# Optimization experiments

Measured on AMD Instinct MI355X. Metric: run time of the kernel, lower is better.

Reference implementation:

```python
import jax, jax.numpy as jnp
import numpy as np
from jax.scipy.linalg import solve_triangular

EPS = 1e-5
CHUNK = 64

def _rms(x, w, eps=EPS):
    return x * jax.lax.rsqrt(jnp.mean(x * x, axis=-1, keepdims=True) + eps) * w

def _l2norm(x, eps=1e-6):
    return x * jax.lax.rsqrt(jnp.sum(x * x, axis=-1, keepdims=True) + eps)

def _causal_conv(x, w):
    # x: [B,T,C], w: [C,K] depthwise causal short conv
    K = w.shape[1]
    T = x.shape[1]
    xp = jnp.pad(x, ((0, 0), (K - 1, 0), (0, 0)))
    return sum(xp[:, j:j + T, :] * w[:, j] for j in range(K))

def _chunk_gated_delta_rule(q, k, v, g, beta, chunk=CHUNK):
    # q,k: [B,H,T,Dk] (l2-normalized, q pre-scaled); v: [B,H,T,Dv]; g,beta: [B,H,T]
    Bb, H, T, Dk = k.shape
    Dv = v.shape[-1]
    N = T // chunk
    qc, kc, vc = (a.reshape(Bb, H, N, chunk, -1) for a in (q, k, v))
    gc = g.reshape(Bb, H, N, chunk)
    bc = beta.reshape(Bb, H, N, chunk)
    gcs = jnp.cumsum(gc, axis=-1)  # within-chunk cumulative log-decay
    tri = jnp.tril(jnp.ones((chunk, chunk), bool))
    tri_s = jnp.tril(jnp.ones((chunk, chunk), bool), -1)
    diff = gcs[..., :, None] - gcs[..., None, :]
    decay = jnp.where(tri, jnp.exp(jnp.where(tri, diff, 0.0)), 0.0)  # [B,H,N,C,C]
    k_beta = kc * bc[..., None]
    v_beta = vc * bc[..., None]
    A = jnp.einsum('bhnck,bhndk->bhncd', k_beta, kc) * decay
    A = jnp.where(tri_s, A, 0.0)
    eye = jnp.eye(chunk, dtype=q.dtype)
    Tmat = solve_triangular(eye + A, jnp.broadcast_to(eye, A.shape), lower=True)  # (I+A)^-1
    u = Tmat @ v_beta                               # [B,H,N,C,Dv]
    w = Tmat @ (k_beta * jnp.exp(gcs)[..., None])   # [B,H,N,C,Dk]

    def step(S, inp):
        q_i, k_i, u_i, w_i, g_i, dm_i = inp
        attn = jnp.where(tri, jnp.einsum('bhck,bhdk->bhcd', q_i, k_i) * dm_i, 0.0)
        v_new = u_i - w_i @ S
        o_i = (q_i * jnp.exp(g_i)[..., None]) @ S + attn @ v_new
        g_last = g_i[..., -1]
        k_dec = k_i * jnp.exp(g_last[..., None] - g_i)[..., None]
        S = S * jnp.exp(g_last)[..., None, None] + jnp.einsum('bhck,bhcv->bhkv', k_dec, v_new)
        return S, o_i

    xs = tuple(jnp.moveaxis(a, 2, 0) for a in (qc, kc, u, w, gcs, decay))
    S0 = jnp.zeros((Bb, H, Dk, Dv), q.dtype)
    _, outs = jax.lax.scan(step, S0, xs)  # [N,B,H,C,Dv]
    return jnp.moveaxis(outs, 0, 2).reshape(Bb, H, T, Dv)

def _layer_forward(x, mask, ln1_w, qkvz_w, ba_w, conv_w, A_log, dt_bias,
                   o_norm_w, out_w, ln2_w, gate_w, up_w, down_w):
    B, T, D = x.shape
    H = A_log.shape[0]
    kd = qkvz_w.shape[0] // 4  # key_dim == value_dim here (k_heads==v_heads, Dk==Dv)
    vd = kd
    Dk = kd // H
    Dv = vd // H
    silu = jax.nn.silu
    h = _rms(x, ln1_w)
    qkvz = h @ qkvz_w.T
    q, k, v, z = jnp.split(qkvz, [kd, 2 * kd, 2 * kd + vd], axis=-1)
    b, a = jnp.split(h @ ba_w.T, 2, axis=-1)  # [B,T,H] each
    mixed = jnp.concatenate([q, k, v], axis=-1) * mask[..., None]
    mixed = silu(_causal_conv(mixed, conv_w))
    q, k, v = jnp.split(mixed, [kd, 2 * kd], axis=-1)
    q = _l2norm(q.reshape(B, T, H, Dk))
    k = _l2norm(k.reshape(B, T, H, Dk))
    v = v.reshape(B, T, H, Dv)
    beta = jax.nn.sigmoid(b) * mask[..., None]
    g = -jnp.exp(A_log) * jax.nn.softplus(a + dt_bias) * mask[..., None]
    scale = Dk ** -0.5
    bhtd = lambda t: jnp.transpose(t, (0, 2, 1, 3))
    o = _chunk_gated_delta_rule(bhtd(q) * scale, bhtd(k), bhtd(v),
                                jnp.transpose(g, (0, 2, 1)), jnp.transpose(beta, (0, 2, 1)))
    o = jnp.transpose(o, (0, 2, 1, 3))  # [B,T,H,Dv]
    o = _rms(o, o_norm_w) * silu(z.reshape(B, T, H, Dv))  # gated RMSNorm
    x = x + o.reshape(B, T, vd) @ out_w.T
    h2 = _rms(x, ln2_w)
    mlp_out = (silu(h2 @ gate_w.T) * (h2 @ up_w.T)) @ down_w.T
    return x + mlp_out

def setup_inputs():
    key = jax.random.key(0)
    ks = jax.random.split(key, 12)
    B, T, D, H, Dk, Dv, M, K = 1, 4096, 2048, 16, 128, 128, 8192, 4
    kd, vd = H * Dk, H * Dv
    nrm = lambda i, shp, sc=0.02: jax.random.normal(ks[i], shp, jnp.float32) * sc
    return {
        'x': nrm(0, (B, T, D), 1.0),
        'mask': jnp.ones((B, T), jnp.float32),
        'ln1_w': jnp.ones((D,), jnp.float32),
        'qkvz_w': nrm(1, (2 * kd + 2 * vd, D)),
        'ba_w': nrm(2, (2 * H, D)),
        'conv_w': nrm(3, (2 * kd + vd, K), 0.3),
        'A_log': jnp.log(jax.random.uniform(ks[4], (H,), jnp.float32, 1.0, 16.0)),
        'dt_bias': nrm(5, (H,), 0.5),
        'o_norm_w': jnp.ones((Dv,), jnp.float32),
        'out_w': nrm(6, (D, vd)),
        'ln2_w': jnp.ones((D,), jnp.float32),
        'gate_w': nrm(7, (M, D)),
        'up_w': nrm(8, (M, D)),
        'down_w': nrm(9, (D, M)),
    }

def reference(x, mask, ln1_w, qkvz_w, ba_w, conv_w, A_log, dt_bias,
              o_norm_w, out_w, ln2_w, gate_w, up_w, down_w):
    return _layer_forward(x, mask, ln1_w, qkvz_w, ba_w, conv_w, A_log, dt_bias,
                          o_norm_w, out_w, ln2_w, gate_w, up_w, down_w)
```

## Files before the change

kernel.cpp:

```cpp
#include <hip/hip_runtime.h>
#include <math.h>

#define T_LEN 4096
#define DMODEL 2048
#define NH 16
#define CQKV 6144
#define CQKVZ 8192
#define SCALE 0.08838834764831845f

using bf16x8 = __attribute__((ext_vector_type(8))) short;
using f32x4  = __attribute__((ext_vector_type(4))) float;

__device__ __forceinline__ float siluf(float x) { return x / (1.0f + __expf(-x)); }

__device__ __forceinline__ unsigned short f2bf(float f) {
  unsigned int u = __float_as_uint(f);
  u = (u + 0x7FFFu + ((u >> 16) & 1u)) >> 16;
  return (unsigned short)u;
}
__device__ __forceinline__ float bf2f(unsigned short u) {
  return __uint_as_float(((unsigned int)u) << 16);
}
__device__ __forceinline__ ushort4 pack4(float a, float b, float c, float d) {
  ushort4 r; r.x = f2bf(a); r.y = f2bf(b); r.z = f2bf(c); r.w = f2bf(d); return r;
}

__device__ __forceinline__ void gl_lds16(const unsigned short* g, unsigned short* l) {
  __builtin_amdgcn_global_load_lds(
      (const __attribute__((address_space(1))) void*)g,
      (__attribute__((address_space(3))) void*)l, 16, 0, 0);
}

template<int MODE>
__global__ __launch_bounds__(256) void rmsnorm_kernel(const float* __restrict__ x,
                                                      const float* __restrict__ w,
                                                      float* __restrict__ outf,
                                                      unsigned short* __restrict__ outb) {
  const int t = blockIdx.x;
  const int tid = threadIdx.x;
  const float4* xr = (const float4*)(x + (size_t)t * DMODEL);
  float4 v0 = xr[tid];
  float4 v1 = xr[tid + 256];
  float s = v0.x*v0.x + v0.y*v0.y + v0.z*v0.z + v0.w*v0.w
          + v1.x*v1.x + v1.y*v1.y + v1.z*v1.z + v1.w*v1.w;
#pragma unroll
  for (int off = 32; off > 0; off >>= 1) s += __shfl_down(s, off);
  __shared__ float red[4];
  if ((tid & 63) == 0) red[tid >> 6] = s;
  __syncthreads();
  const float tot = red[0] + red[1] + red[2] + red[3];
  const float r = rsqrtf(tot * (1.0f / DMODEL) + 1e-5f);
  const float4* wr = (const float4*)w;
  const float4 w0 = wr[tid], w1 = wr[tid + 256];
  float4 o0, o1;
  o0.x = v0.x*r*w0.x; o0.y = v0.y*r*w0.y; o0.z = v0.z*r*w0.z; o0.w = v0.w*r*w0.w;
  o1.x = v1.x*r*w1.x; o1.y = v1.y*r*w1.y; o1.z = v1.z*r*w1.z; o1.w = v1.w*r*w1.w;
  if (MODE == 1) {
    float4* orow = (float4*)(outf + (size_t)t * DMODEL);
    orow[tid] = o0;
    orow[tid + 256] = o1;
  }
  ushort4* brow = (ushort4*)(outb + (size_t)t * DMODEL);
  brow[tid] = pack4(o0.x, o0.y, o0.z, o0.w);
  brow[tid + 256] = pack4(o1.x, o1.y, o1.z, o1.w);
}

__global__ __launch_bounds__(256) void f2b_kernel(const float* __restrict__ in,
                                                  unsigned short* __restrict__ out) {
  const size_t i = (size_t)blockIdx.x * 256 + threadIdx.x;
  const float4 a = ((const float4*)in)[2 * i];
  const float4 b = ((const float4*)in)[2 * i + 1];
  ((ushort4*)out)[2 * i] = pack4(a.x, a.y, a.z, a.w);
  ((ushort4*)out)[2 * i + 1] = pack4(b.x, b.y, b.z, b.w);
}

template<int EPI>
__global__ __launch_bounds__(512, 2) void gemm8p_kernel(const unsigned short* __restrict__ A,
                                                        const unsigned short* __restrict__ B,
                                                        float* __restrict__ Cf,
                                                        unsigned short* __restrict__ Cb,
                                                        unsigned short* __restrict__ Zb,
                                                        int M, int N, int K) {
  __shared__ __align__(16) unsigned short lds[8][8192];
  const int nbm = M >> 8, nbn = N >> 8, nwg = nbm * nbn;
  const int nt = K >> 6;
  int bmi, bni;
  {
    const int bid = blockIdx.x;
    const int cpx = nwg >> 3;
    int sc = 1;
    while (sc * sc < cpx) sc <<= 1;
    if (sc * sc > cpx) sc >>= 1;
    const int scn = (sc > 0) ? (cpx / sc) : 0;
    if ((nwg & 7) == 0 && sc > 0 && sc * scn == cpx && (nbm % sc) == 0 && (nbn % scn) == 0) {
      const int chunk = bid & 7, widx = bid >> 3;
      const int regc = nbn / scn;
      bmi = (chunk / regc) * sc + widx / scn;
      bni = (chunk % regc) * scn + widx % scn;
    } else {
      bmi = bid / nbn; bni = bid % nbn;
    }
  }
  const int bm = bmi << 8, bn = bni << 8;
  const int tid = threadIdx.x;
  const int wv = tid >> 6, ln = tid & 63;
  const int fr = ln & 15, qq = ln >> 4;
  const int wm = wv >> 2, wn = wv & 3;
  const int rsw = (fr >> 1) & 3;
  const int s_sl = (ln & 3) ^ ((ln >> 3) & 3);

  f32x4 acc[8][4];
  const f32x4 zero = {0.f, 0.f, 0.f, 0.f};
#pragma unroll
  for (int mf = 0; mf < 8; mf++)
#pragma unroll
    for (int nf = 0; nf < 4; nf++) acc[mf][nf] = zero;

  bf16x8 afr[8], bfr[2];

  auto stage_half = [&](int t2, int part) {
    if (t2 >= nt) return;
    const unsigned short* Mat = (part >= 2) ? B : A;
    const int gb = (part >= 2) ? bn : bm;
    const int kk = part & 1;
    const int slot = ((t2 & 1) << 2) | part;
    const int k0 = t2 * 64 + kk * 32;
#pragma unroll
    for (int q = 0; q < 2; q++) {
      gl_lds16(Mat + (size_t)(gb + wv * 32 + q * 16 + (ln >> 2)) * K + k0 + s_sl * 8,
               &lds[slot][(wv * 32 + q * 16) * 32]);
    }
  };
  auto lda = [&](int tb, int kk) {
#pragma unroll
    for (int mf = 0; mf < 8; mf++) {
      const int ar = wm * 128 + mf * 16 + fr;
      afr[mf] = *(const bf16x8*)&lds[tb | kk][ar * 32 + ((qq ^ rsw) << 3)];
    }
  };
  auto ldb = [&](int tb, int kk, int nh) {
#pragma unroll
    for (int nj = 0; nj < 2; nj++) {
      const int br = wn * 64 + (nh * 2 + nj) * 16 + fr;
      bfr[nj] = *(const bf16x8*)&lds[tb | (2 + kk)][br * 32 + ((qq ^ rsw) << 3)];
    }
  };
  auto mm = [&](int nh) {
    __builtin_amdgcn_s_setprio(1);
#pragma unroll
    for (int mf = 0; mf < 8; mf++)
#pragma unroll
      for (int nj = 0; nj < 2; nj++)
        acc[mf][nh * 2 + nj] =
            __builtin_amdgcn_mfma_f32_16x16x32_bf16(afr[mf], bfr[nj], acc[mf][nh * 2 + nj], 0, 0, 0);
    __builtin_amdgcn_s_setprio(0);
  };

  stage_half(0, 0); stage_half(0, 2); stage_half(0, 1); stage_half(0, 3);
  stage_half(1, 0); stage_half(1, 2);
  asm volatile("s_waitcnt vmcnt(4)" ::: "memory");
  __builtin_amdgcn_s_barrier();
  asm volatile("" ::: "memory");

  for (int t = 0; t < nt; t++) {
    const int tb = (t & 1) << 2;
    lda(tb, 0); ldb(tb, 0, 0);
    stage_half(t + 1, 1);
    __builtin_amdgcn_s_barrier();
    mm(0);
    __builtin_amdgcn_s_barrier();
    ldb(tb, 0, 1);
    stage_half(t + 1, 3);
    __builtin_amdgcn_s_barrier();
    mm(1);
    __builtin_amdgcn_s_barrier();
    lda(tb, 1); ldb(tb, 1, 1);
    stage_half(t + 2, 0);
    __builtin_amdgcn_s_barrier();
    mm(1);
    __builtin_amdgcn_s_barrier();
    ldb(tb, 1, 0);
    stage_half(t + 2, 2);
    __builtin_amdgcn_s_barrier();
    mm(0);
    if (t + 1 < nt) {
      asm volatile("s_waitcnt lgkmcnt(0)" ::: "memory");
      __builtin_amdgcn_sched_barrier(0);
      if (t == nt - 2) {
        asm volatile("s_waitcnt vmcnt(0)" ::: "memory");
      } else {
        asm volatile("s_waitcnt vmcnt(4)" ::: "memory");
      }
      __builtin_amdgcn_sched_barrier(0);
      __builtin_amdgcn_s_barrier();
      __builtin_amdgcn_sched_barrier(0);
    }
  }

  const int cm4 = qq * 4;
  if (EPI == 3) {
    const int bn2 = bn >> 1;
#pragma unroll
    for (int mf = 0; mf < 8; mf++) {
#pragma unroll
      for (int p = 0; p < 2; p++) {
#pragma unroll
        for (int r = 0; r < 4; r++) {
          const int grow = bm + wm * 128 + mf * 16 + cm4 + r;
          const int gcol = bn2 + wn * 32 + p * 16 + fr;
          Cb[(size_t)grow * 8192 + gcol] =
              f2bf(siluf(acc[mf][2 * p][r]) * acc[mf][2 * p + 1][r]);
        }
      }
    }
  } else {
    const bool isZ = (Zb != nullptr) && (bn >= CQKV);
#pragma unroll
    for (int mf = 0; mf < 8; mf++) {
#pragma unroll
      for (int nf = 0; nf < 4; nf++) {
#pragma unroll
        for (int r = 0; r < 4; r++) {
          const int grow = bm + wm * 128 + mf * 16 + cm4 + r;
          const int gcol = bn + wn * 64 + nf * 16 + fr;
          const float v = acc[mf][nf][r];
          if (EPI == 0) {
            const unsigned short bv = f2bf(v);
            if (isZ) Zb[(size_t)grow * 2048 + (gcol - CQKV)] = bv;
            else     Cb[(size_t)grow * N + gcol] = bv;
          } else {
            Cf[(size_t)grow * N + gcol] += v;
          }
        }
      }
    }
  }
}

template<int EPI, int BM, int BN>
__global__ __launch_bounds__(512, 4) void gemm256_kernel(const unsigned short* __restrict__ A,
                                                         const unsigned short* __restrict__ B,
                                                         float* __restrict__ Cf,
                                                         const float* __restrict__ Xres,
                                                         int M, int N, int K) {
  constexpr int MI = 4;
  constexpr int NI = BN / 64;
  constexpr int AW = BM / 128;
  constexpr int BW = BN / 128;
  __shared__ __align__(16) unsigned short lds[3][(BM + BN) * 32];
  const int nbm = M / BM, nbn = N / BN, nwg = nbm * nbn;
  const int nt = K >> 5;
  int bmi, bni;
  {
    const int bid = blockIdx.x;
    const int cpx = nwg >> 3;
    int sc = 1;
    while (sc * sc < cpx) sc <<= 1;
    if (sc * sc > cpx) sc >>= 1;
    const int scn = (sc > 0) ? (cpx / sc) : 0;
    if ((nwg & 7) == 0 && sc > 0 && sc * scn == cpx && (nbm % sc) == 0 && (nbn % scn) == 0) {
      const int chunk = bid & 7, widx = bid >> 3;
      const int regc = nbn / scn;
      bmi = (chunk / regc) * sc + widx / scn;
      bni = (chunk % regc) * scn + widx % scn;
    } else {
      bmi = bid / nbn; bni = bid % nbn;
    }
  }
  const int bm = bmi * BM, bn = bni * BN;
  const int tid = threadIdx.x;
  const int wv = tid >> 6, ln = tid & 63;
  const int fr = ln & 15, qq = ln >> 4;
  const int wm = wv >> 2, wn = wv & 3;
  const int ra0 = wm * 64, rb0 = wn * (BN / 4);
  const int lrow = ln >> 2;
  const int lslot = ln & 3;

  f32x4 acc[MI][NI];
  const f32x4 zero = {0.f, 0.f, 0.f, 0.f};
#pragma unroll
  for (int mi = 0; mi < MI; mi++)
#pragma unroll
    for (int ni = 0; ni < NI; ni++) acc[mi][ni] = zero;

  auto stage = [&](int buf, int t) {
    const int k0 = t << 5;
#pragma unroll
    for (int q = 0; q < AW; q++) {
      const int lr = q * 128 + wv * 16 + lrow;
      const int sl = lslot ^ ((lr >> 1) & 3);
      gl_lds16(A + (size_t)(bm + lr) * K + k0 + sl * 8,
               &lds[buf][(q * 128 + wv * 16) * 32]);
    }
#pragma unroll
    for (int q = 0; q < BW; q++) {
      const int lr = q * 128 + wv * 16 + lrow;
      const int sl = lslot ^ ((lr >> 1) & 3);
      gl_lds16(B + (size_t)(bn + lr) * K + k0 + sl * 8,
               &lds[buf][BM * 32 + (q * 128 + wv * 16) * 32]);
    }
  };

  stage(0, 0);
  stage(1, 1);
  asm volatile("s_waitcnt vmcnt(%0)" :: "i"(AW + BW) : "memory");
  __builtin_amdgcn_s_barrier();
  asm volatile("" ::: "memory");

  for (int t = 0; t < nt; t++) {
    const int cb = t % 3;
    const int b2 = (t + 2) % 3;
    const unsigned short* lA = &lds[cb][0];
    const unsigned short* lB = &lds[cb][BM * 32];
    bf16x8 bfr[NI];
#pragma unroll
    for (int ni = 0; ni < NI; ni++) {
      const int r = rb0 + ni * 16 + fr;
      bfr[ni] = *(const bf16x8*)&lB[r * 32 + ((qq ^ ((r >> 1) & 3)) << 3)];
    }
    bf16x8 afr[MI];
#pragma unroll
    for (int mi = 0; mi < MI; mi++) {
      const int r = ra0 + mi * 16 + fr;
      afr[mi] = *(const bf16x8*)&lA[r * 32 + ((qq ^ ((r >> 1) & 3)) << 3)];
    }
    if (t + 2 < nt) stage(b2, t + 2);
    __builtin_amdgcn_s_setprio(1);
#pragma unroll
    for (int mi = 0; mi < MI; mi++)
#pragma unroll
      for (int ni = 0; ni < NI; ni++)
        acc[mi][ni] = __builtin_amdgcn_mfma_f32_16x16x32_bf16(afr[mi], bfr[ni], acc[mi][ni], 0, 0, 0);
    __builtin_amdgcn_s_setprio(0);
    if (t + 1 < nt) {
      asm volatile("s_waitcnt lgkmcnt(0)" ::: "memory");
      if (t + 2 < nt) {
        asm volatile("s_waitcnt vmcnt(%0)" :: "i"(AW + BW) : "memory");
      } else {
        asm volatile("s_waitcnt vmcnt(0)" ::: "memory");
      }
      __builtin_amdgcn_s_barrier();
      asm volatile("" ::: "memory");
    }
  }

  const int cm4 = qq * 4;
#pragma unroll
  for (int mi = 0; mi < MI; mi++) {
#pragma unroll
    for (int ni = 0; ni < NI; ni++) {
#pragma unroll
      for (int r = 0; r < 4; r++) {
        const int grow = bm + ra0 + mi * 16 + cm4 + r;
        const int gcol = bn + rb0 + ni * 16 + fr;
        const size_t off = (size_t)grow * N + gcol;
        const float v = acc[mi][ni][r];
        if (EPI == 1) {
          Cf[off] += v;
        } else {
          Cf[off] = Xres[off] + v;
        }
      }
    }
  }
}

__global__ __launch_bounds__(256) void ba_gemm_kernel(const unsigned short* __restrict__ h_in,
                                                      const float* __restrict__ ba_w,
                                                      float* __restrict__ ba_out) {
  __shared__ __align__(16) float hl[2048];
  __shared__ float red[32][9];
  const int t = blockIdx.x;
  const int tid = threadIdx.x;
  union { uint4 u; unsigned short s[8]; } wv_;
  wv_.u = *(const uint4*)(h_in + (size_t)t * DMODEL + tid * 8);
#pragma unroll
  for (int j = 0; j < 8; j++) hl[tid * 8 + j] = bf2f(wv_.s[j]);
  __syncthreads();
  const int c = tid & 31;
  const int p = tid >> 5;
  const float* wrow = ba_w + (size_t)c * DMODEL + p * 256;
  const float* hrow = hl + p * 256;
  float s = 0.f;
#pragma unroll 8
  for (int k = 0; k < 256; k++) s += hrow[k] * wrow[k];
  red[c][p] = s;
  __syncthreads();
  if (tid < 32) {
    float tot = 0.f;
#pragma unroll
    for (int q = 0; q < 8; q++) tot += red[tid][q];
    ba_out[(size_t)t * 32 + tid] = tot;
  }
}

__global__ __launch_bounds__(256) void conv_norm_kernel(const unsigned short* __restrict__ qkvz,
                                                        const float* __restrict__ conv_w,
                                                        const float* __restrict__ mask,
                                                        unsigned short* __restrict__ mixed) {
  __shared__ float vals[6144];
  const int t = blockIdx.x;
  const int tid = threadIdx.x;
  float mj[4];
#pragma unroll
  for (int j = 0; j < 4; j++) {
    const int tt = t - 3 + j;
    mj[j] = (tt >= 0) ? mask[tt] : 0.f;
  }
#pragma unroll
  for (int p = 0; p < 6; p++) {
    const int c4 = (p * 256 + tid) * 4;
    const float4 w0 = *(const float4*)(conv_w + (size_t)c4 * 4);
    const float4 w1 = *(const float4*)(conv_w + (size_t)c4 * 4 + 4);
    const float4 w2 = *(const float4*)(conv_w + (size_t)c4 * 4 + 8);
    const float4 w3 = *(const float4*)(conv_w + (size_t)c4 * 4 + 12);
    const float wj0[4] = {w0.x, w0.y, w0.z, w0.w};
    const float wj1[4] = {w1.x, w1.y, w1.z, w1.w};
    const float wj2[4] = {w2.x, w2.y, w2.z, w2.w};
    const float wj3[4] = {w3.x, w3.y, w3.z, w3.w};
    float4 acc = make_float4(0.f, 0.f, 0.f, 0.f);
#pragma unroll
    for (int j = 0; j < 4; j++) {
      const int tt = t - 3 + j;
      if (tt < 0) continue;
      const ushort4 xb = *(const ushort4*)(qkvz + (size_t)tt * CQKVZ + c4);
      acc.x += bf2f(xb.x) * mj[j] * wj0[j];
      acc.y += bf2f(xb.y) * mj[j] * wj1[j];
      acc.z += bf2f(xb.z) * mj[j] * wj2[j];
      acc.w += bf2f(xb.w) * mj[j] * wj3[j];
    }
    vals[c4]     = siluf(acc.x);
    vals[c4 + 1] = siluf(acc.y);
    vals[c4 + 2] = siluf(acc.z);
    vals[c4 + 3] = siluf(acc.w);
  }
  __syncthreads();
  unsigned short* orow = mixed + (size_t)t * CQKV;
  const int hh = tid >> 3;
  const int li = tid & 7;
  const int base = hh * 128 + li * 16;
  float loc[16];
  float s = 0.f;
#pragma unroll
  for (int j = 0; j < 16; j++) { loc[j] = vals[base + j]; s += loc[j] * loc[j]; }
#pragma unroll
  for (int msk = 1; msk < 8; msk <<= 1) s += __shfl_xor(s, msk);
  const float rn = rsqrtf(s + 1e-6f);
#pragma unroll
  for (int j8 = 0; j8 < 2; j8++) {
    *(ushort4*)(orow + base + j8 * 8) =
        pack4(loc[j8*8+0]*rn, loc[j8*8+1]*rn, loc[j8*8+2]*rn, loc[j8*8+3]*rn);
    *(ushort4*)(orow + base + j8 * 8 + 4) =
        pack4(loc[j8*8+4]*rn, loc[j8*8+5]*rn, loc[j8*8+6]*rn, loc[j8*8+7]*rn);
  }
  const int vc = 4096 + tid * 8;
  *(ushort4*)(orow + vc) = pack4(vals[vc], vals[vc+1], vals[vc+2], vals[vc+3]);
  *(ushort4*)(orow + vc + 4) = pack4(vals[vc+4], vals[vc+5], vals[vc+6], vals[vc+7]);
}

__global__ __launch_bounds__(256) void beta_g_kernel(const float* __restrict__ ba,
                                                     const float* __restrict__ A_log,
                                                     const float* __restrict__ dt_bias,
                                                     const float* __restrict__ mask,
                                                     float* __restrict__ beta,
                                                     float* __restrict__ g) {
  const int idx = blockIdx.x * 256 + threadIdx.x;
  const int t = idx >> 4;
  const int h = idx & 15;
  const float b = ba[(size_t)t * 32 + h];
  const float a = ba[(size_t)t * 32 + 16 + h];
  const float m = mask[t];
  beta[idx] = m / (1.0f + expf(-b));
  const float xx = a + dt_bias[h];
  const float sp = (xx > 20.0f) ? xx : log1pf(expf(xx));
  g[idx] = -expf(A_log[h]) * sp * m;
}

__global__ __launch_bounds__(256) void gcs_kernel(const float* __restrict__ g,
                                                  float* __restrict__ gcsbuf,
                                                  float* __restrict__ edkbuf,
                                                  float* __restrict__ egqbuf,
                                                  float* __restrict__ adecbuf) {
  const int idx = blockIdx.x * 256 + threadIdx.x;
  if (idx >= 1024) return;
  const int h = idx >> 6;
  const int n = idx & 63;
  const int t0 = n * 64;
  float s = 0.f;
  for (int i = 0; i < 64; i++) {
    s += g[(size_t)(t0 + i) * NH + h];
    gcsbuf[(size_t)idx * 64 + i] = s;
  }
  const float glast = s;
  adecbuf[idx] = __expf(glast);
  for (int i = 0; i < 64; i++) {
    const float gi = gcsbuf[(size_t)idx * 64 + i];
    edkbuf[(size_t)idx * 64 + i] = __expf(glast - gi);
    egqbuf[(size_t)idx * 64 + i] = __expf(gi) * SCALE;
  }
}

__global__ __launch_bounds__(256) void pre_attn_kernel(const unsigned short* __restrict__ mixed,
                                                       const float* __restrict__ gcsbuf,
                                                       const float* __restrict__ betabuf,
                                                       float* __restrict__ abuf,
                                                       unsigned short* __restrict__ attnb) {
  __shared__ __align__(16) unsigned short kbl[64 * 128];
  __shared__ __align__(16) unsigned short qbl[64 * 128];
  __shared__ float gcs_s[64];
  __shared__ float betal[64];
  const int blk = blockIdx.x;
  const int h = blk >> 6;
  const int n = blk & 63;
  const int t0 = n * 64;
  const int tid = threadIdx.x;
  if (tid < 64) {
    gcs_s[tid] = gcsbuf[(size_t)blk * 64 + tid];
    betal[tid] = betabuf[(size_t)(t0 + tid) * NH + h];
  }
#pragma unroll
  for (int p = 0; p < 4; p++) {
    const int idx = tid + p * 256;
    const int i = idx >> 4, dg = idx & 15;
    *(uint4*)&kbl[i * 128 + ((dg ^ (i & 7)) << 3)] =
        *(const uint4*)(mixed + (size_t)(t0 + i) * CQKV + 2048 + h * 128 + dg * 8);
    *(uint4*)&qbl[i * 128 + ((dg ^ (i & 7)) << 3)] =
        *(const uint4*)(mixed + (size_t)(t0 + i) * CQKV + h * 128 + dg * 8);
  }
  __syncthreads();
  const int ln = tid & 63;
  const int wv = tid >> 6;
  const int fr = ln & 15;
  const int g = ln >> 4;
  const int i0 = wv * 16;
  f32x4 accA[4], accQ[4];
  const f32x4 zero = {0.f, 0.f, 0.f, 0.f};
#pragma unroll
  for (int jt = 0; jt < 4; jt++) { accA[jt] = zero; accQ[jt] = zero; }
#pragma unroll
  for (int ks = 0; ks < 4; ks++) {
    const int kb = ks * 4 + g;
    const int ar = i0 + fr;
    const bf16x8 aK = *(const bf16x8*)&kbl[ar * 128 + ((kb ^ (ar & 7)) << 3)];
    const bf16x8 aQ = *(const bf16x8*)&qbl[ar * 128 + ((kb ^ (ar & 7)) << 3)];
#pragma unroll
    for (int jt = 0; jt < 4; jt++) {
      const int br = jt * 16 + fr;
      const bf16x8 b = *(const bf16x8*)&kbl[br * 128 + ((kb ^ (br & 7)) << 3)];
      accA[jt] = __builtin_amdgcn_mfma_f32_16x16x32_bf16(aK, b, accA[jt], 0, 0, 0);
      accQ[jt] = __builtin_amdgcn_mfma_f32_16x16x32_bf16(aQ, b, accQ[jt], 0, 0, 0);
    }
  }
#pragma unroll
  for (int jt = 0; jt < 4; jt++) {
    const int j = jt * 16 + fr;
    const float gj = gcs_s[j];
#pragma unroll
    for (int r = 0; r < 4; r++) {
      const int i = i0 + g * 4 + r;
      const float gi = gcs_s[i];
      const float dec = __expf(fminf(gi - gj, 0.f));
      abuf[(size_t)blk * 4096 + i * 64 + j] = (i > j) ? accA[jt][r] * betal[i] * dec : 0.f;
      attnb[(size_t)blk * 4096 + i * 64 + j] =
          f2bf((i >= j) ? accQ[jt][r] * dec * SCALE : 0.f);
    }
  }
}

__global__ __launch_bounds__(256) void pre_solve_kernel(const float* __restrict__ abuf,
                                                        const float* __restrict__ betabuf,
                                                        float* __restrict__ tbuf) {
  __shared__ float Al[64][65];
  __shared__ float Tl[64][65];
  const int blk = blockIdx.x;
  const int h = blk >> 6;
  const int n = blk & 63;
  const int t0 = n * 64;
  const int tid = threadIdx.x;
#pragma unroll
  for (int rep = 0; rep < 4; rep++) {
    const int lin = rep * 256 + tid;
    const int i = lin >> 4;
    const int j = (lin & 15) * 4;
    const float4 av = *(const float4*)(abuf + (size_t)blk * 4096 + i * 64 + j);
    Al[i][j] = av.x; Al[i][j + 1] = av.y; Al[i][j + 2] = av.z; Al[i][j + 3] = av.w;
  }
  __syncthreads();
  if (tid < 64) {
    const int j = tid;
    const float bj = betabuf[(size_t)(t0 + j) * NH + h];
    for (int i = 0; i < 64; i++) {
      float s = (i == j) ? 1.0f : 0.0f;
      for (int l = j; l < i; l++) s -= Al[i][l] * Tl[l][j];
      Tl[i][j] = s;
    }
    for (int i = j; i < 64; i++) Tl[i][j] *= bj;
  }
  __syncthreads();
#pragma unroll
  for (int rep = 0; rep < 4; rep++) {
    const int lin = rep * 256 + tid;
    const int i = lin >> 4;
    const int j = (lin & 15) * 4;
    float4 tv;
    tv.x = Tl[i][j]; tv.y = Tl[i][j + 1]; tv.z = Tl[i][j + 2]; tv.w = Tl[i][j + 3];
    *(float4*)(tbuf + (size_t)blk * 4096 + i * 64 + j) = tv;
  }
}

__global__ __launch_bounds__(256) void pre_uw_kernel(const unsigned short* __restrict__ mixed,
                                                     const float* __restrict__ tbuf,
                                                     const float* __restrict__ gcsbuf,
                                                     unsigned short* __restrict__ ubf,
                                                     unsigned short* __restrict__ wbf) {
  __shared__ __align__(16) float Tl[64][68];
  __shared__ __align__(16) float xl[64][132];
  __shared__ float egcs[64];
  const int blk = blockIdx.x;
  const int h = blk >> 6;
  const int n = blk & 63;
  const int t0 = n * 64;
  const int tid = threadIdx.x;
  if (tid < 64) egcs[tid] = __expf(gcsbuf[(size_t)blk * 64 + tid]);
#pragma unroll
  for (int rep = 0; rep < 4; rep++) {
    const int lin = rep * 256 + tid;
    const int i = lin >> 4;
    const int j = (lin & 15) * 4;
    const float4 tv = *(const float4*)(tbuf + (size_t)blk * 4096 + i * 64 + j);
    *(float4*)&Tl[i][j] = tv;
  }
#pragma unroll
  for (int rep = 0; rep < 4; rep++) {
    const int lin = rep * 256 + tid;
    const int i = lin >> 4;
    const int d8 = (lin & 15) * 8;
    union { uint4 u; unsigned short s[8]; } w;
    w.u = *(const uint4*)(mixed + (size_t)(t0 + i) * CQKV + 4096 + h * 128 + d8);
#pragma unroll
    for (int j = 0; j < 8; j++) xl[i][d8 + j] = bf2f(w.s[j]);
  }
  __syncthreads();
  const int cgu = tid & 15;
  const int riu = tid >> 4;
  const int i0 = riu * 4;
  const int d0 = cgu * 8;
  float acc[4][8];
#pragma unroll
  for (int a = 0; a < 4; a++)
#pragma unroll
    for (int b = 0; b < 8; b++) acc[a][b] = 0.f;
#pragma unroll 2
  for (int j = 0; j < 64; j++) {
    const float tv[4] = {Tl[i0][j], Tl[i0 + 1][j], Tl[i0 + 2][j], Tl[i0 + 3][j]};
    const float4 x0 = *(const float4*)&xl[j][d0];
    const float4 x1 = *(const float4*)&xl[j][d0 + 4];
    const float xv[8] = {x0.x, x0.y, x0.z, x0.w, x1.x, x1.y, x1.z, x1.w};
#pragma unroll
    for (int a = 0; a < 4; a++)
#pragma unroll
      for (int b = 0; b < 8; b++) acc[a][b] += tv[a] * xv[b];
  }
#pragma unroll
  for (int b = 0; b < 8; b++) {
    *(ushort4*)(ubf + (size_t)blk * 8192 + riu * 512 + (size_t)(d0 + b) * 4) =
        pack4(acc[0][b], acc[1][b], acc[2][b], acc[3][b]);
  }
  __syncthreads();
#pragma unroll
  for (int rep = 0; rep < 4; rep++) {
    const int lin = rep * 256 + tid;
    const int i = lin >> 4;
    const int d8 = (lin & 15) * 8;
    union { uint4 u; unsigned short s[8]; } w;
    w.u = *(const uint4*)(mixed + (size_t)(t0 + i) * CQKV + 2048 + h * 128 + d8);
    const float e = egcs[i];
#pragma unroll
    for (int j = 0; j < 8; j++) xl[i][d8 + j] = bf2f(w.s[j]) * e;
  }
  __syncthreads();
#pragma unroll
  for (int a = 0; a < 4; a++)
#pragma unroll
    for (int b = 0; b < 8; b++) acc[a][b] = 0.f;
#pragma unroll 2
  for (int j = 0; j < 64; j++) {
    const float tv[4] = {Tl[i0][j], Tl[i0 + 1][j], Tl[i0 + 2][j], Tl[i0 + 3][j]};
    const float4 x0 = *(const float4*)&xl[j][d0];
    const float4 x1 = *(const float4*)&xl[j][d0 + 4];
    const float xv[8] = {x0.x, x0.y, x0.z, x0.w, x1.x, x1.y, x1.z, x1.w};
#pragma unroll
    for (int a = 0; a < 4; a++)
#pragma unroll
      for (int b = 0; b < 8; b++) acc[a][b] += tv[a] * xv[b];
  }
#pragma unroll
  for (int a = 0; a < 4; a++) {
    const int l = i0 + a;
    unsigned short* wp = wbf + (size_t)(t0 + l) * 2048 + h * 128 + ((cgu ^ (l & 7)) << 3);
    *(ushort4*)wp = pack4(-acc[a][0], -acc[a][1], -acc[a][2], -acc[a][3]);
    *(ushort4*)(wp + 4) = pack4(-acc[a][4], -acc[a][5], -acc[a][6], -acc[a][7]);
  }
}

__global__ __launch_bounds__(256) void ktrans_kernel(const unsigned short* __restrict__ mixed,
                                                     const float* __restrict__ edkbuf,
                                                     const float* __restrict__ egqbuf,
                                                     unsigned short* __restrict__ kdT,
                                                     unsigned short* __restrict__ qe) {
  __shared__ __align__(16) float kl[64][132];
  __shared__ float edk_s[64];
  __shared__ float egq_s[64];
  const int blk = blockIdx.x;
  const int h = blk >> 6;
  const int n = blk & 63;
  const int t0 = n * 64;
  const int tid = threadIdx.x;
  if (tid < 64) {
    edk_s[tid] = edkbuf[(size_t)blk * 64 + tid];
    egq_s[tid] = egqbuf[(size_t)blk * 64 + tid];
  }
#pragma unroll
  for (int q = 0; q < 4; q++) {
    const int idx = tid + q * 256;
    const int l = idx >> 4, d8 = (idx & 15) * 8;
    union { uint4 u; unsigned short s[8]; } w;
    w.u = *(const uint4*)(mixed + (size_t)(t0 + l) * CQKV + 2048 + h * 128 + d8);
#pragma unroll
    for (int j = 0; j < 8; j++) kl[l][d8 + j] = bf2f(w.s[j]);
  }
  __syncthreads();
#pragma unroll
  for (int q = 0; q < 4; q++) {
    const int idx = tid + q * 256;
    const int d = idx >> 3, lsl = idx & 7;
    const int l8 = lsl * 8;
    float v[8];
#pragma unroll
    for (int j = 0; j < 8; j++) v[j] = kl[l8 + j][d] * edk_s[l8 + j];
    unsigned short* p = kdT + (size_t)blk * 8192 + d * 64 + ((lsl ^ (d & 7)) << 3);
    *(ushort4*)p = pack4(v[0], v[1], v[2], v[3]);
    *(ushort4*)(p + 4) = pack4(v[4], v[5], v[6], v[7]);
  }
#pragma unroll
  for (int q = 0; q < 4; q++) {
    const int idx = tid + q * 256;
    const int i = idx >> 4, c8 = (idx & 15) * 8;
    union { uint4 u; unsigned short s[8]; } w;
    w.u = *(const uint4*)(mixed + (size_t)(t0 + i) * CQKV + h * 128 + c8);
    const float e = egq_s[i];
    unsigned short* qp = qe + (size_t)(t0 + i) * 2048 + h * 128 + c8;
    *(ushort4*)qp = pack4(bf2f(w.s[0]) * e, bf2f(w.s[1]) * e, bf2f(w.s[2]) * e, bf2f(w.s[3]) * e);
    *(ushort4*)(qp + 4) = pack4(bf2f(w.s[4]) * e, bf2f(w.s[5]) * e, bf2f(w.s[6]) * e, bf2f(w.s[7]) * e);
  }
}

__global__ __launch_bounds__(512, 1) void scan_kernel(const unsigned short* __restrict__ wbf,
                                                      const unsigned short* __restrict__ kdT,
                                                      const unsigned short* __restrict__ ubf,
                                                      const float* __restrict__ adecbuf,
                                                      unsigned short* __restrict__ STb,
                                                      unsigned short* __restrict__ vtb,
                                                      const float* __restrict__ gw,
                                                      const float* __restrict__ uw,
                                                      const float* __restrict__ dw,
                                                      const float* __restrict__ ow,
                                                      unsigned short* __restrict__ Wgu,
                                                      unsigned short* __restrict__ Wd,
                                                      unsigned short* __restrict__ Wo) {
  __shared__ __align__(16) unsigned short stage[2][16384];
  __shared__ __align__(16) unsigned short privAll[4][3072];
  if (blockIdx.x >= 32) {
    const int xb = blockIdx.x - 32;
    const int tid = threadIdx.x;
    if (xb < 8192) {
      const bool isUp = (xb >= 4096);
      const float* src = isUp ? uw : gw;
      const size_t e = ((size_t)(isUp ? xb - 4096 : xb) * 512 + tid) * 8;
      const int r = (int)(e >> 11);
      const int col = (int)(e & 2047);
      const int drow = (r >> 4) * 32 + (r & 15) + (isUp ? 16 : 0);
      const float4 a = *(const float4*)(src + e);
      const float4 b = *(const float4*)(src + e + 4);
      unsigned short* dst = Wgu + (size_t)drow * 2048 + col;
      *(ushort4*)dst = pack4(a.x, a.y, a.z, a.w);
      *(ushort4*)(dst + 4) = pack4(b.x, b.y, b.z, b.w);
    } else {
      const float* src; unsigned short* dst; size_t u;
      if (xb < 12288) { src = dw; dst = Wd; u = (size_t)(xb - 8192) * 512 + tid; }
      else            { src = ow; dst = Wo; u = (size_t)(xb - 12288) * 512 + tid; }
      const float4 a = ((const float4*)src)[2 * u];
      const float4 b = ((const float4*)src)[2 * u + 1];
      ((ushort4*)dst)[2 * u] = pack4(a.x, a.y, a.z, a.w);
      ((ushort4*)dst)[2 * u + 1] = pack4(b.x, b.y, b.z, b.w);
    }
    return;
  }
  const int h = blockIdx.x >> 1;
  const int chalf = blockIdx.x & 1;
  const int tid = threadIdx.x;
  const int wv = tid >> 6;
  if (wv >= 4) {
    __builtin_amdgcn_s_barrier();
    for (int n = 0; n < 63; n++) __builtin_amdgcn_s_barrier();
    return;
  }
  const int ln = tid & 63;
  const int fr = ln & 15;
  const int g  = ln >> 4;
  const int c0 = chalf * 64 + wv * 16;
  const int fsw = fr & 7;
  unsigned short* privA = &privAll[wv][0];
  unsigned short* privB = &privAll[wv][2048];
  const f32x4 zero = {0.f, 0.f, 0.f, 0.f};

  f32x4 acc2[8];
#pragma unroll
  for (int dt = 0; dt < 8; dt++) acc2[dt] = zero;

  auto stage_wk = [&](int buf, int n1) {
    const int t0n = n1 * 64;
    const size_t kbase = (size_t)(h * 64 + n1) * 8192;
#pragma unroll
    for (int q = 0; q < 4; q++) {
      const int m = wv * 4 + q;
      gl_lds16(wbf + (size_t)(t0n + m * 4 + (ln >> 4)) * 2048 + h * 128 + (ln & 15) * 8,
               &stage[buf][m * 512]);
      gl_lds16(kdT + kbase + (m * 8 + (ln >> 3)) * 64 + (ln & 7) * 8,
               &stage[buf][8192 + m * 512]);
    }
  };

  ushort4 ur4[4];
#pragma unroll
  for (int lt = 0; lt < 4; lt++)
    ur4[lt] = *(const ushort4*)(ubf + (size_t)(h * 64) * 8192 + (lt * 4 + g) * 512 + (c0 + fr) * 4);
  float ad = adecbuf[h * 64];
  stage_wk(0, 0);
  asm volatile("s_waitcnt vmcnt(0)" ::: "memory");
  __builtin_amdgcn_s_barrier();
  asm volatile("" ::: "memory");

  for (int n = 0; n < 64; n++) {
    const int blk = h * 64 + n;
    const unsigned short* wl = &stage[n & 1][0];
    const unsigned short* kl = &stage[n & 1][8192];
    if (n + 1 < 64) stage_wk((n + 1) & 1, n + 1);
    __builtin_amdgcn_sched_barrier(0);
    ushort4 ur4n[4];
    float adn = 0.f;
    if (n + 1 < 64) {
      const size_t ub = (size_t)(blk + 1) * 8192;
#pragma unroll
      for (int lt = 0; lt < 4; lt++)
        ur4n[lt] = *(const ushort4*)(ubf + ub + (lt * 4 + g) * 512 + (c0 + fr) * 4);
      adn = adecbuf[blk + 1];
    } else {
#pragma unroll
      for (int lt = 0; lt < 4; lt++) { ur4n[lt].x = 0; ur4n[lt].y = 0; ur4n[lt].z = 0; ur4n[lt].w = 0; }
    }
    __builtin_amdgcn_sched_barrier(0);
#pragma unroll
    for (int dt = 0; dt < 8; dt++) {
      const int slot = dt * 2 + (g >> 1);
      const ushort4 pv = pack4(acc2[dt][0], acc2[dt][1], acc2[dt][2], acc2[dt][3]);
      *(ushort4*)&privA[fr * 128 + ((slot ^ fsw) << 3) + (g & 1) * 4] = pv;
      *(ushort4*)(STb + (size_t)blk * 16384 + (dt * 4 + g) * 512 + (c0 + fr) * 4) = pv;
    }
    f32x4 acc1[4];
#pragma unroll
    for (int lt = 0; lt < 4; lt++) {
      f32x4 t;
      t[0] = bf2f(ur4[lt].x); t[1] = bf2f(ur4[lt].y);
      t[2] = bf2f(ur4[lt].z); t[3] = bf2f(ur4[lt].w);
      acc1[lt] = t;
    }
#pragma unroll
    for (int ks = 0; ks < 4; ks++) {
      const int kb = ks * 4 + g;
      const bf16x8 b = *(const bf16x8*)&privA[fr * 128 + ((kb ^ fsw) << 3)];
#pragma unroll
      for (int lt = 0; lt < 4; lt++) {
        const bf16x8 a = *(const bf16x8*)&wl[(lt * 16 + fr) * 128 + ((kb ^ fsw) << 3)];
        acc1[lt] = __builtin_amdgcn_mfma_f32_16x16x32_bf16(a, b, acc1[lt], 0, 0, 0);
      }
    }
#pragma unroll
    for (int lt = 0; lt < 4; lt++) {
      const int slot = lt * 2 + (g >> 1);
      const ushort4 pv = pack4(acc1[lt][0], acc1[lt][1], acc1[lt][2], acc1[lt][3]);
      *(ushort4*)&privB[fr * 64 + ((slot ^ fsw) << 3) + (g & 1) * 4] = pv;
      *(ushort4*)(vtb + (size_t)blk * 8192 + (lt * 4 + g) * 512 + (c0 + fr) * 4) = pv;
    }
#pragma unroll
    for (int dt = 0; dt < 8; dt++) {
      acc2[dt][0] *= ad; acc2[dt][1] *= ad; acc2[dt][2] *= ad; acc2[dt][3] *= ad;
    }
#pragma unroll
    for (int ks = 0; ks < 2; ks++) {
      const int kb = ks * 4 + g;
      const bf16x8 b = *(const bf16x8*)&privB[fr * 64 + ((kb ^ fsw) << 3)];
#pragma unroll
      for (int dt = 0; dt < 8; dt++) {
        const bf16x8 a = *(const bf16x8*)&kl[(dt * 16 + fr) * 64 + ((kb ^ fsw) << 3)];
        acc2[dt] = __builtin_amdgcn_mfma_f32_16x16x32_bf16(a, b, acc2[dt], 0, 0, 0);
      }
    }
#pragma unroll
    for (int lt = 0; lt < 4; lt++) ur4[lt] = ur4n[lt];
    ad = adn;
    if (n + 1 < 64) {
      asm volatile("s_waitcnt lgkmcnt(0)" ::: "memory");
      __builtin_amdgcn_sched_barrier(0);
      asm volatile("s_waitcnt vmcnt(17)" ::: "memory");
      __builtin_amdgcn_sched_barrier(0);
      __builtin_amdgcn_s_barrier();
      __builtin_amdgcn_sched_barrier(0);
    }
  }
}

__global__ __launch_bounds__(256) void ocomp_kernel(const unsigned short* __restrict__ qe,
                                                    const unsigned short* __restrict__ STbuf,
                                                    const unsigned short* __restrict__ vtbuf,
                                                    const unsigned short* __restrict__ attnb,
                                                    const unsigned short* __restrict__ zb,
                                                    const float* __restrict__ onw,
                                                    unsigned short* __restrict__ ob) {
  __shared__ __align__(16) unsigned short STl[128 * 128];
  __shared__ __align__(16) unsigned short vtl[128 * 64];
  __shared__ __align__(16) unsigned short ql[64 * 128];
  __shared__ __align__(16) unsigned short al[64 * 64];
  const int blk = blockIdx.x;
  const int h = blk >> 6;
  const int n = blk & 63;
  const int t0 = n * 64;
  const int tid = threadIdx.x;
#pragma unroll
  for (int q = 0; q < 8; q++) {
    const int o = tid + q * 256;
    const int dq = o >> 6, w = o & 63;
    const uint4 v = *(const uint4*)(STbuf + (size_t)blk * 16384 + (size_t)o * 8);
    const int cA = 2 * w, cB = 2 * w + 1;
    uint2 h0; h0.x = v.x; h0.y = v.y;
    uint2 h1; h1.x = v.z; h1.y = v.w;
    *(uint2*)&STl[cA * 128 + (((dq >> 1) ^ (cA & 7)) << 3) + (dq & 1) * 4] = h0;
    *(uint2*)&STl[cB * 128 + (((dq >> 1) ^ (cB & 7)) << 3) + (dq & 1) * 4] = h1;
  }
#pragma unroll
  for (int q = 0; q < 4; q++) {
    const int o = tid + q * 256;
    const int lq = o >> 6, w = o & 63;
    const uint4 v = *(const uint4*)(vtbuf + (size_t)blk * 8192 + (size_t)o * 8);
    const int cA = 2 * w, cB = 2 * w + 1;
    uint2 h0; h0.x = v.x; h0.y = v.y;
    uint2 h1; h1.x = v.z; h1.y = v.w;
    *(uint2*)&vtl[cA * 64 + (((lq >> 1) ^ (cA & 7)) << 3) + (lq & 1) * 4] = h0;
    *(uint2*)&vtl[cB * 64 + (((lq >> 1) ^ (cB & 7)) << 3) + (lq & 1) * 4] = h1;
  }
#pragma unroll
  for (int q = 0; q < 4; q++) {
    const int idx = tid + q * 256;
    const int i = idx >> 4, dg = idx & 15;
    *(uint4*)&ql[i * 128 + ((dg ^ (i & 7)) << 3)] =
        *(const uint4*)(qe + (size_t)(t0 + i) * 2048 + h * 128 + dg * 8);
  }
#pragma unroll
  for (int q = 0; q < 2; q++) {
    const int idx = tid + q * 256;
    const int i = idx >> 3, lsl = idx & 7;
    *(uint4*)&al[i * 64 + ((lsl ^ (i & 7)) << 3)] =
        *(const uint4*)(attnb + (size_t)blk * 4096 + i * 64 + lsl * 8);
  }
  __syncthreads();
  const int ln = tid & 63;
  const int wv = tid >> 6;
  const int fr = ln & 15;
  const int g = ln >> 4;
  const int i0 = wv * 16;
  f32x4 acc[8];
  const f32x4 zero = {0.f, 0.f, 0.f, 0.f};
#pragma unroll
  for (int nt = 0; nt < 8; nt++) acc[nt] = zero;
#pragma unroll
  for (int ks = 0; ks < 4; ks++) {
    const int kb = ks * 4 + g;
    const int ar = i0 + fr;
    const bf16x8 a = *(const bf16x8*)&ql[ar * 128 + ((kb ^ (ar & 7)) << 3)];
#pragma unroll
    for (int nt = 0; nt < 8; nt++) {
      const int c = nt * 16 + fr;
      const bf16x8 b = *(const bf16x8*)&STl[c * 128 + ((kb ^ (c & 7)) << 3)];
      acc[nt] = __builtin_amdgcn_mfma_f32_16x16x32_bf16(a, b, acc[nt], 0, 0, 0);
    }
  }
#pragma unroll
  for (int ks = 0; ks < 2; ks++) {
    const int kb = ks * 4 + g;
    const int ar = i0 + fr;
    const bf16x8 a = *(const bf16x8*)&al[ar * 64 + ((kb ^ (ar & 7)) << 3)];
#pragma unroll
    for (int nt = 0; nt < 8; nt++) {
      const int c = nt * 16 + fr;
      const bf16x8 b = *(const bf16x8*)&vtl[c * 64 + ((kb ^ (c & 7)) << 3)];
      acc[nt] = __builtin_amdgcn_mfma_f32_16x16x32_bf16(a, b, acc[nt], 0, 0, 0);
    }
  }
  float s0 = 0.f, s1 = 0.f, s2 = 0.f, s3 = 0.f;
#pragma unroll
  for (int nt = 0; nt < 8; nt++) {
    s0 += acc[nt][0] * acc[nt][0];
    s1 += acc[nt][1] * acc[nt][1];
    s2 += acc[nt][2] * acc[nt][2];
    s3 += acc[nt][3] * acc[nt][3];
  }
#pragma unroll
  for (int m = 1; m < 16; m <<= 1) {
    s0 += __shfl_xor(s0, m);
    s1 += __shfl_xor(s1, m);
    s2 += __shfl_xor(s2, m);
    s3 += __shfl_xor(s3, m);
  }
  float rn[4];
  rn[0] = rsqrtf(s0 * (1.0f / 128.0f) + 1e-5f);
  rn[1] = rsqrtf(s1 * (1.0f / 128.0f) + 1e-5f);
  rn[2] = rsqrtf(s2 * (1.0f / 128.0f) + 1e-5f);
  rn[3] = rsqrtf(s3 * (1.0f / 128.0f) + 1e-5f);
#pragma unroll
  for (int nt = 0; nt < 8; nt++) {
    const int c = nt * 16 + fr;
    const float wn = onw[c];
#pragma unroll
    for (int r = 0; r < 4; r++) {
      const size_t off = (size_t)(t0 + i0 + g * 4 + r) * 2048 + h * 128 + c;
      const float zz = siluf(bf2f(zb[off]));
      ob[off] = f2bf(acc[nt][r] * rn[r] * wn * zz);
    }
  }
}

extern "C" void kernel_launch(void* const* d_in, const int* in_sizes, int n_in,
                              void* d_out, int out_size, void* d_ws, size_t ws_size,
                              hipStream_t stream) {
  (void)in_sizes; (void)n_in; (void)out_size;
  const float* x        = (const float*)d_in[0];
  const float* mask     = (const float*)d_in[1];
  const float* ln1_w    = (const float*)d_in[2];
  const float* qkvz_w   = (const float*)d_in[3];
  const float* ba_w     = (const float*)d_in[4];
  const float* conv_w   = (const float*)d_in[5];
  const float* A_log    = (const float*)d_in[6];
  const float* dt_bias  = (const float*)d_in[7];
  const float* o_norm_w = (const float*)d_in[8];
  const float* out_w    = (const float*)d_in[9];
  const float* ln2_w    = (const float*)d_in[10];
  const float* gate_w   = (const float*)d_in[11];
  const float* up_w     = (const float*)d_in[12];
  const float* down_w   = (const float*)d_in[13];
  float* out = (float*)d_out;

  const size_t NEED_BYTES = (size_t)75825152 * 4;
  if (ws_size < NEED_BYTES) return;

  float* ws = (float*)d_ws;
  unsigned short* mixed_bf = (unsigned short*)ws;
  unsigned short* Wgu = (unsigned short*)ws;
  unsigned short* Wd = (unsigned short*)(ws + 16777216);
  unsigned short* qkvz_bf = (unsigned short*)(ws + 25165824);
  unsigned short* u_bf = (unsigned short*)(ws + 25165824);
  unsigned short* wbf = (unsigned short*)(ws + 33554432);
  unsigned short* kdT = (unsigned short*)(ws + 37748736);
  unsigned short* comb_bf = (unsigned short*)(ws + 25165824);
  unsigned short* z_bf = (unsigned short*)(ws + 41943040);
  float* a_buf = ws + 46137344;
  unsigned short* vt_buf = (unsigned short*)(ws + 46137344);
  float* t_buf = ws + 50331648;
  unsigned short* qe_bf = (unsigned short*)(ws + 50331648);
  unsigned short* h_bf  = (unsigned short*)(ws + 54525952);
  unsigned short* ob    = (unsigned short*)(ws + 54525952);
  unsigned short* h2_bf = (unsigned short*)(ws + 54525952);
  unsigned short* attn_bf = (unsigned short*)(ws + 58720256);
  unsigned short* Wq = (unsigned short*)(ws + 62914560);
  unsigned short* ST_buf = (unsigned short*)(ws + 62914560);
  unsigned short* Wo = (unsigned short*)(ws + 71303168);
  float* ba_buf   = ws + 73400320;
  float* beta_buf = ws + 73531392;
  float* g_buf    = ws + 73596928;
  float* gcs_buf  = ws + 73662464;
  float* edk_buf  = ws + 73728000;
  float* egq_buf  = ws + 73793536;
  float* adec_buf = ws + 73859072;

  rmsnorm_kernel<2><<<4096, 256, 0, stream>>>(x, ln1_w, nullptr, h_bf);
  f2b_kernel<<<8192, 256, 0, stream>>>(qkvz_w, Wq);
  gemm8p_kernel<0><<<512, 512, 0, stream>>>(h_bf, Wq, nullptr, qkvz_bf, z_bf, 4096, 8192, 2048);
  ba_gemm_kernel<<<4096, 256, 0, stream>>>(h_bf, ba_w, ba_buf);
  conv_norm_kernel<<<4096, 256, 0, stream>>>(qkvz_bf, conv_w, mask, mixed_bf);
  beta_g_kernel<<<256, 256, 0, stream>>>(ba_buf, A_log, dt_bias, mask, beta_buf, g_buf);
  gcs_kernel<<<4, 256, 0, stream>>>(g_buf, gcs_buf, edk_buf, egq_buf, adec_buf);
  pre_attn_kernel<<<1024, 256, 0, stream>>>(mixed_bf, gcs_buf, beta_buf, a_buf, attn_bf);
  pre_solve_kernel<<<1024, 256, 0, stream>>>(a_buf, beta_buf, t_buf);
  pre_uw_kernel<<<1024, 256, 0, stream>>>(mixed_bf, t_buf, gcs_buf, u_bf, wbf);
  ktrans_kernel<<<1024, 256, 0, stream>>>(mixed_bf, edk_buf, egq_buf, kdT, qe_bf);
  scan_kernel<<<13344, 512, 0, stream>>>(wbf, kdT, u_bf, adec_buf, ST_buf, vt_buf,
                                         gate_w, up_w, down_w, out_w,
                                         Wgu, Wd, Wo);
  ocomp_kernel<<<1024, 256, 0, stream>>>(qe_bf, ST_buf, vt_buf, attn_bf,
                                         z_bf, o_norm_w, ob);
  gemm256_kernel<4, 128, 128><<<512, 512, 0, stream>>>(ob, Wo, out, x, 4096, 2048, 2048);
  rmsnorm_kernel<2><<<4096, 256, 0, stream>>>(out, ln2_w, nullptr, h2_bf);
  gemm8p_kernel<3><<<1024, 512, 0, stream>>>(h2_bf, Wgu, nullptr, comb_bf, nullptr, 4096, 16384, 2048);
  gemm256_kernel<1, 128, 128><<<512, 512, 0, stream>>>(comb_bf, Wd, out, nullptr, 4096, 2048, 8192);
}
```

Before: 1.214 ms.

## Fuse triangular solve into u/w kernel and split scan across four blocks per head

```diff
diff --git a/kernel.cpp b/kernel.cpp
--- a/kernel.cpp
+++ b/kernel.cpp
@@ -567,54 +567,14 @@
   }
 }
 
-__global__ __launch_bounds__(256) void pre_solve_kernel(const float* __restrict__ abuf,
-                                                        const float* __restrict__ betabuf,
-                                                        float* __restrict__ tbuf) {
-  __shared__ float Al[64][65];
-  __shared__ float Tl[64][65];
-  const int blk = blockIdx.x;
-  const int h = blk >> 6;
-  const int n = blk & 63;
-  const int t0 = n * 64;
-  const int tid = threadIdx.x;
-#pragma unroll
-  for (int rep = 0; rep < 4; rep++) {
-    const int lin = rep * 256 + tid;
-    const int i = lin >> 4;
-    const int j = (lin & 15) * 4;
-    const float4 av = *(const float4*)(abuf + (size_t)blk * 4096 + i * 64 + j);
-    Al[i][j] = av.x; Al[i][j + 1] = av.y; Al[i][j + 2] = av.z; Al[i][j + 3] = av.w;
-  }
-  __syncthreads();
-  if (tid < 64) {
-    const int j = tid;
-    const float bj = betabuf[(size_t)(t0 + j) * NH + h];
-    for (int i = 0; i < 64; i++) {
-      float s = (i == j) ? 1.0f : 0.0f;
-      for (int l = j; l < i; l++) s -= Al[i][l] * Tl[l][j];
-      Tl[i][j] = s;
-    }
-    for (int i = j; i < 64; i++) Tl[i][j] *= bj;
-  }
-  __syncthreads();
-#pragma unroll
-  for (int rep = 0; rep < 4; rep++) {
-    const int lin = rep * 256 + tid;
-    const int i = lin >> 4;
-    const int j = (lin & 15) * 4;
-    float4 tv;
-    tv.x = Tl[i][j]; tv.y = Tl[i][j + 1]; tv.z = Tl[i][j + 2]; tv.w = Tl[i][j + 3];
-    *(float4*)(tbuf + (size_t)blk * 4096 + i * 64 + j) = tv;
-  }
-}
-
-__global__ __launch_bounds__(256) void pre_uw_kernel(const unsigned short* __restrict__ mixed,
-                                                     const float* __restrict__ tbuf,
-                                                     const float* __restrict__ gcsbuf,
-                                                     unsigned short* __restrict__ ubf,
-                                                     unsigned short* __restrict__ wbf) {
+__global__ __launch_bounds__(256) void pre_suw_kernel(const unsigned short* __restrict__ mixed,
+                                                      const float* __restrict__ abuf,
+                                                      const float* __restrict__ gcsbuf,
+                                                      const float* __restrict__ betabuf,
+                                                      unsigned short* __restrict__ ubf,
+                                                      unsigned short* __restrict__ wbf) {
   __shared__ __align__(16) float Tl[64][68];
-  __shared__ __align__(16) float xl[64][132];
+  __shared__ __align__(16) union { float A[64][65]; float x[64][132]; } U;
   __shared__ float egcs[64];
   const int blk = blockIdx.x;
   const int h = blk >> 6;
@@ -627,9 +587,21 @@
     const int lin = rep * 256 + tid;
     const int i = lin >> 4;
     const int j = (lin & 15) * 4;
-    const float4 tv = *(const float4*)(tbuf + (size_t)blk * 4096 + i * 64 + j);
-    *(float4*)&Tl[i][j] = tv;
-  }
+    const float4 av = *(const float4*)(abuf + (size_t)blk * 4096 + i * 64 + j);
+    U.A[i][j] = av.x; U.A[i][j + 1] = av.y; U.A[i][j + 2] = av.z; U.A[i][j + 3] = av.w;
+  }
+  __syncthreads();
+  if (tid < 64) {
+    const int j = tid;
+    const float bj = betabuf[(size_t)(t0 + j) * NH + h];
+    for (int i = 0; i < 64; i++) {
+      float s = (i == j) ? 1.0f : 0.0f;
+      for (int l = j; l < i; l++) s -= U.A[i][l] * Tl[l][j];
+      Tl[i][j] = s;
+    }
+    for (int i = j; i < 64; i++) Tl[i][j] *= bj;
+  }
+  __syncthreads();
 #pragma unroll
   for (int rep = 0; rep < 4; rep++) {
     const int lin = rep * 256 + tid;
@@ -638,7 +610,7 @@
     union { uint4 u; unsigned short s[8]; } w;
     w.u = *(const uint4*)(mixed + (size_t)(t0 + i) * CQKV + 4096 + h * 128 + d8);
 #pragma unroll
-    for (int j = 0; j < 8; j++) xl[i][d8 + j] = bf2f(w.s[j]);
+    for (int j = 0; j < 8; j++) U.x[i][d8 + j] = bf2f(w.s[j]);
   }
   __syncthreads();
   const int cgu = tid & 15;
@@ -653,8 +625,8 @@
 #pragma unroll 2
   for (int j = 0; j < 64; j++) {
     const float tv[4] = {Tl[i0][j], Tl[i0 + 1][j], Tl[i0 + 2][j], Tl[i0 + 3][j]};
-    const float4 x0 = *(const float4*)&xl[j][d0];
-    const float4 x1 = *(const float4*)&xl[j][d0 + 4];
+    const float4 x0 = *(const float4*)&U.x[j][d0];
+    const float4 x1 = *(const float4*)&U.x[j][d0 + 4];
     const float xv[8] = {x0.x, x0.y, x0.z, x0.w, x1.x, x1.y, x1.z, x1.w};
 #pragma unroll
     for (int a = 0; a < 4; a++)
@@ -676,7 +648,7 @@
     w.u = *(const uint4*)(mixed + (size_t)(t0 + i) * CQKV + 2048 + h * 128 + d8);
     const float e = egcs[i];
 #pragma unroll
-    for (int j = 0; j < 8; j++) xl[i][d8 + j] = bf2f(w.s[j]) * e;
+    for (int j = 0; j < 8; j++) U.x[i][d8 + j] = bf2f(w.s[j]) * e;
   }
   __syncthreads();
 #pragma unroll
@@ -686,8 +658,8 @@
 #pragma unroll 2
   for (int j = 0; j < 64; j++) {
     const float tv[4] = {Tl[i0][j], Tl[i0 + 1][j], Tl[i0 + 2][j], Tl[i0 + 3][j]};
-    const float4 x0 = *(const float4*)&xl[j][d0];
-    const float4 x1 = *(const float4*)&xl[j][d0 + 4];
+    const float4 x0 = *(const float4*)&U.x[j][d0];
+    const float4 x1 = *(const float4*)&U.x[j][d0 + 4];
     const float xv[8] = {x0.x, x0.y, x0.z, x0.w, x1.x, x1.y, x1.z, x1.w};
 #pragma unroll
     for (int a = 0; a < 4; a++)
@@ -769,9 +741,9 @@
                                                       unsigned short* __restrict__ Wd,
                                                       unsigned short* __restrict__ Wo) {
   __shared__ __align__(16) unsigned short stage[2][16384];
-  __shared__ __align__(16) unsigned short privAll[4][3072];
-  if (blockIdx.x >= 32) {
-    const int xb = blockIdx.x - 32;
+  __shared__ __align__(16) unsigned short privAll[2][3072];
+  if (blockIdx.x >= 64) {
+    const int xb = blockIdx.x - 64;
     const int tid = threadIdx.x;
     if (xb < 8192) {
       const bool isUp = (xb >= 4096);
@@ -796,11 +768,11 @@
     }
     return;
   }
-  const int h = blockIdx.x >> 1;
-  const int chalf = blockIdx.x & 1;
+  const int h = blockIdx.x >> 2;
+  const int qu = blockIdx.x & 3;
   const int tid = threadIdx.x;
   const int wv = tid >> 6;
-  if (wv >= 4) {
+  if (wv >= 2) {
     __builtin_amdgcn_s_barrier();
     for (int n = 0; n < 63; n++) __builtin_amdgcn_s_barrier();
     return;
@@ -808,7 +780,7 @@
   const int ln = tid & 63;
   const int fr = ln & 15;
   const int g  = ln >> 4;
-  const int c0 = chalf * 64 + wv * 16;
+  const int c0 = qu * 32 + wv * 16;
   const int fsw = fr & 7;
   unsigned short* privA = &privAll[wv][0];
   unsigned short* privB = &privAll[wv][2048];
@@ -822,8 +794,8 @@
     const int t0n = n1 * 64;
     const size_t kbase = (size_t)(h * 64 + n1) * 8192;
 #pragma unroll
-    for (int q = 0; q < 4; q++) {
-      const int m = wv * 4 + q;
+    for (int q = 0; q < 8; q++) {
+      const int m = wv * 8 + q;
       gl_lds16(wbf + (size_t)(t0n + m * 4 + (ln >> 4)) * 2048 + h * 128 + (ln & 15) * 8,
                &stage[buf][m * 512]);
       gl_lds16(kdT + kbase + (m * 8 + (ln >> 3)) * 64 + (ln & 7) * 8,
@@ -1074,7 +1046,6 @@
   unsigned short* z_bf = (unsigned short*)(ws + 41943040);
   float* a_buf = ws + 46137344;
   unsigned short* vt_buf = (unsigned short*)(ws + 46137344);
-  float* t_buf = ws + 50331648;
   unsigned short* qe_bf = (unsigned short*)(ws + 50331648);
   unsigned short* h_bf  = (unsigned short*)(ws + 54525952);
   unsigned short* ob    = (unsigned short*)(ws + 54525952);
@@ -1099,10 +1070,9 @@
   beta_g_kernel<<<256, 256, 0, stream>>>(ba_buf, A_log, dt_bias, mask, beta_buf, g_buf);
   gcs_kernel<<<4, 256, 0, stream>>>(g_buf, gcs_buf, edk_buf, egq_buf, adec_buf);
   pre_attn_kernel<<<1024, 256, 0, stream>>>(mixed_bf, gcs_buf, beta_buf, a_buf, attn_bf);
-  pre_solve_kernel<<<1024, 256, 0, stream>>>(a_buf, beta_buf, t_buf);
-  pre_uw_kernel<<<1024, 256, 0, stream>>>(mixed_bf, t_buf, gcs_buf, u_bf, wbf);
+  pre_suw_kernel<<<1024, 256, 0, stream>>>(mixed_bf, a_buf, gcs_buf, beta_buf, u_bf, wbf);
   ktrans_kernel<<<1024, 256, 0, stream>>>(mixed_bf, edk_buf, egq_buf, kdT, qe_bf);
-  scan_kernel<<<13344, 512, 0, stream>>>(wbf, kdT, u_bf, adec_buf, ST_buf, vt_buf,
+  scan_kernel<<<13376, 512, 0, stream>>>(wbf, kdT, u_bf, adec_buf, ST_buf, vt_buf,
                                          gate_w, up_w, down_w, out_w,
                                          Wgu, Wd, Wo);
   ocomp_kernel<<<1024, 256, 0, stream>>>(qe_bf, ST_buf, vt_buf, attn_bf,
```

New measurement: 1.316 ms. +8.4%, slower.
